# Kernel tuning notes

Hardware: AMD Instinct MI355X
Metric: run time of the kernel (lower is better)

Reference implementation:

```python
import jax, jax.numpy as jnp
import numpy as np
from jax import lax

T = 100
TAU = 2.0
ALPHA = 2.0  # ATan surrogate default
EPS = 1e-5

@jax.custom_vjp
def atan_spike(x):
    return (x >= 0.0).astype(x.dtype)

def _atan_fwd(x):
    return atan_spike(x), x

def _atan_bwd(x, g):
    return (g * (ALPHA / 2.0) / (1.0 + (jnp.pi / 2.0 * ALPHA * x) ** 2),)

atan_spike.defvjp(_atan_fwd, _atan_bwd)

def lif(x_seq):
    # spikingjelly LIFNode: decay_input=True, v_threshold=1, hard reset to 0
    def step(v, x):
        v = v + (x - v) / TAU
        s = atan_spike(v - 1.0)
        return v * (1.0 - s), s
    return lax.scan(step, jnp.zeros_like(x_seq[0]), x_seq)[1]

def conv3x3(x, w):
    return lax.conv_general_dilated(x, w, (1, 1), 'SAME',
                                    dimension_numbers=('NCHW', 'OIHW', 'NCHW'))

def bn(x, g, b, m, v):
    inv = g / jnp.sqrt(v + EPS)
    return x * inv[:, None, None] + (b - m * inv)[:, None, None]

def maxpool2(x):
    return lax.reduce_window(x, -jnp.inf, lax.max, (1, 1, 2, 2), (1, 1, 2, 2), 'VALID')

def setup_inputs() -> dict:
    key = jax.random.key(0)
    ks = jax.random.split(key, 10)
    B, C = 16, 64
    x = jax.random.uniform(ks[0], (B, 1, 28, 28), dtype=jnp.float32)
    W1 = jax.random.normal(ks[1], (C, 1, 3, 3), dtype=jnp.float32) * np.sqrt(2.0 / 9)
    W2 = jax.random.normal(ks[2], (C, C, 3, 3), dtype=jnp.float32) * np.sqrt(2.0 / (9 * C))
    Wfc1 = jax.random.normal(ks[3], (C * 16, C * 49), dtype=jnp.float32) * np.sqrt(2.0 / (C * 49))
    Wfc2 = jax.random.normal(ks[4], (10, C * 16), dtype=jnp.float32) * np.sqrt(2.0 / (C * 16))
    g1 = jnp.ones((C,), jnp.float32); b1 = jnp.zeros((C,), jnp.float32)
    m1 = jax.random.normal(ks[5], (C,), jnp.float32) * 0.1
    v1 = jax.random.uniform(ks[6], (C,), jnp.float32, 0.5, 1.5)
    g2 = jnp.ones((C,), jnp.float32); b2 = jnp.zeros((C,), jnp.float32)
    m2 = jax.random.normal(ks[7], (C,), jnp.float32) * 0.1
    v2 = jax.random.uniform(ks[8], (C,), jnp.float32, 0.5, 1.5)
    return {'x': x, 'W1': W1, 'g1': g1, 'b1': b1, 'm1': m1, 'v1': v1,
            'W2': W2, 'g2': g2, 'b2': b2, 'm2': m2, 'v2': v2,
            'Wfc1': Wfc1, 'Wfc2': Wfc2}

def reference(x, W1, g1, b1, m1, v1, W2, g2, b2, m2, v2, Wfc1, Wfc2):
    B = x.shape[0]
    C = W1.shape[0]
    # conv1+BN1: input identical at every timestep, compute once and broadcast
    h1 = bn(conv3x3(x, W1), g1, b1, m1, v1)                 # [B,C,28,28]
    x_seq = jnp.broadcast_to(h1, (T,) + h1.shape)           # [T,B,C,28,28]
    s1 = lif(x_seq)                                         # [T,B,C,28,28]
    p1 = maxpool2(s1.reshape(T * B, C, 28, 28))             # [T*B,C,14,14]
    h2 = bn(conv3x3(p1, W2), g2, b2, m2, v2).reshape(T, B, C, 14, 14)
    s2 = lif(h2)                                            # [T,B,C,14,14]
    p2 = maxpool2(s2.reshape(T * B, C, 14, 14)).reshape(T, B, C * 49)
    s3 = lif(jnp.einsum('tbi,oi->tbo', p2, Wfc1))           # [T,B,C*16]
    s4 = lif(jnp.einsum('tbi,oi->tbo', s3, Wfc2))           # [T,B,10]
    return s4.mean(axis=0)                                  # [B,10]
```

## Files before the change

### kernel.cpp

```cpp
#include <hip/hip_runtime.h>
#include <hip/hip_bf16.h>

typedef unsigned int uint;
typedef _Float16 f16;
typedef _Float16 f16x8 __attribute__((ext_vector_type(8)));
typedef float f32x4 __attribute__((ext_vector_type(4)));

#define T_STEPS 100

#define OFF_H1    (size_t)0
#define OFF_WHI   (size_t)0
#define OFF_WLO   (size_t)73728
#define OFF_P1    (size_t)3211264
#define OFF_H2    (size_t)29425664
#define OFF_H3    (size_t)29425664
#define OFF_S3    (size_t)35979264
#define OFF_H4    (size_t)37617664
#define OFF_WF1L  (size_t)37681664
#define OFF_P2    (size_t)109707264
#define OFF_WF1H  (size_t)114724864

__device__ __forceinline__ int lif_step_i(float& v, float x) {
  v = __fadd_rn(v, __fmul_rn(__fsub_rn(x, v), 0.5f));
  if (v >= 1.0f) { v = 0.0f; return 1; }
  return 0;
}

__global__ __launch_bounds__(256) void k_prep_w2(const float* __restrict__ w2,
                                                 f16* __restrict__ whi, f16* __restrict__ wlo) {
  int i = blockIdx.x * 256 + threadIdx.x;
  int j = i & 7, l = (i >> 3) & 63, cb = (i >> 9) & 3, kb = i >> 11;
  int k = kb * 32 + (l >> 4) * 8 + j;
  int co = cb * 16 + (l & 15);
  int ci = k & 63, tap = k >> 6;
  int dy = tap / 3, dx = tap - 3 * dy;
  float w = w2[((co * 64 + ci) * 3 + dy) * 3 + dx];
  float hif = (fabsf(w) < 6.104e-5f) ? 0.0f : (float)(f16)w;
  whi[i] = (f16)hif;
  wlo[i] = (f16)((w - hif) * 4096.0f);
}

__global__ __launch_bounds__(256) void k_prep_wfc1(const float* __restrict__ wfc1,
                                                   f16* __restrict__ whi, f16* __restrict__ wlo) {
  int i = blockIdx.x * 256 + threadIdx.x;
  int j = i & 7, lane = (i >> 3) & 63;
  int rest = i >> 9;
  int oblk = rest & 63, kbG = rest >> 6;
  int o = oblk * 16 + (lane & 15);
  int k = kbG * 32 + (lane >> 4) * 8 + j;
  float w = wfc1[(size_t)o * 3136 + k];
  float hif = (fabsf(w) < 6.104e-5f) ? 0.0f : (float)(f16)w;
  whi[i] = (f16)hif;
  wlo[i] = (f16)((w - hif) * 4096.0f);
}

__global__ __launch_bounds__(256) void k_zero_h3(float4* __restrict__ p) {
  p[blockIdx.x * 256 + threadIdx.x] = make_float4(0.f, 0.f, 0.f, 0.f);
}

__global__ __launch_bounds__(256) void k_conv1(const float* __restrict__ x, const float* __restrict__ w1,
                                               const float* __restrict__ g1, const float* __restrict__ b1,
                                               const float* __restrict__ m1, const float* __restrict__ v1,
                                               float* __restrict__ h1) {
  int i = blockIdx.x * 256 + threadIdx.x;
  int pos = i % 784;
  int bc  = i / 784;
  int c = bc & 63, b = bc >> 6;
  int y = pos / 28, xx = pos % 28;
  float a = 0.f;
#pragma unroll
  for (int dy = 0; dy < 3; ++dy) {
    int iy = y + dy - 1;
#pragma unroll
    for (int dx = 0; dx < 3; ++dx) {
      int ix = xx + dx - 1;
      if (iy >= 0 && iy < 28 && ix >= 0 && ix < 28)
        a = fmaf(w1[c * 9 + dy * 3 + dx], x[b * 784 + iy * 28 + ix], a);
    }
  }
  float inv  = g1[c] / sqrtf(v1[c] + 1e-5f);
  float bias = __fsub_rn(b1[c], __fmul_rn(m1[c], inv));
  h1[i] = __fadd_rn(__fmul_rn(a, inv), bias);
}

__global__ __launch_bounds__(256) void k_lif1pool(const float* __restrict__ h1,
                                                  unsigned char* __restrict__ p1) {
  int t = blockIdx.x * 256 + threadIdx.x;
  int ci = t & 63, xx = (t >> 6) & 15, y = (t >> 10) & 15, b = t >> 14;
  int pix = y * 16 + xx;
  size_t outbase = (size_t)b * 16384 + pix * 64 + ci;
  const size_t tstride = (size_t)16 * 16384;
  if (y == 0 || y == 15 || xx == 0 || xx == 15) {
    for (int tt = 0; tt < T_STEPS; ++tt) p1[outbase + (size_t)tt * tstride] = 0;
    return;
  }
  int py = y - 1, px = xx - 1;
  const float* hp = h1 + ((size_t)(b * 64 + ci) * 28 + 2 * py) * 28 + 2 * px;
  float h00 = hp[0], h01 = hp[1], h10 = hp[28], h11 = hp[29];
  float v00 = 0.f, v01 = 0.f, v10 = 0.f, v11 = 0.f;
  for (int tt = 0; tt < T_STEPS; ++tt) {
    int s = 0;
    s |= lif_step_i(v00, h00);
    s |= lif_step_i(v01, h01);
    s |= lif_step_i(v10, h10);
    s |= lif_step_i(v11, h11);
    p1[outbase + (size_t)tt * tstride] = (unsigned char)s;
  }
}

__global__ __launch_bounds__(256, 2) void k_conv2(const unsigned char* __restrict__ p1,
                                                  const f16* __restrict__ whi, const f16* __restrict__ wlo,
                                                  const float* __restrict__ g2, const float* __restrict__ b2,
                                                  const float* __restrict__ m2, const float* __restrict__ v2,
                                                  float* __restrict__ h2) {
  __shared__ unsigned char smem[33024];
  const int tid = threadIdx.x;
  const int tb = blockIdx.x;
  const unsigned char* img = p1 + (size_t)tb * 16384;
#pragma unroll
  for (int it = 0; it < 4; ++it) {
    int s = it * 256 + tid;
    uint4 d = *(const uint4*)(img + (size_t)s * 16);
    int pix = s >> 2, c4 = s & 3;
    uint dw[4] = {d.x, d.y, d.z, d.w};
    f16x8 va, vb;
#pragma unroll
    for (int e = 0; e < 8; ++e) {
      va[e] = (f16)(float)((dw[e >> 2] >> ((e & 3) * 8)) & 255u);
      vb[e] = (f16)(float)((dw[2 + (e >> 2)] >> ((e & 3) * 8)) & 255u);
    }
    int rowbase = pix * 128;
    int sw = (pix & 7) << 4;
    *(f16x8*)(smem + rowbase + ((c4 * 32) ^ sw)) = va;
    *(f16x8*)(smem + rowbase + ((c4 * 32 + 16) ^ sw)) = vb;
  }
  if (tid < 16) *(uint4*)(smem + 32768 + tid * 16) = make_uint4(0u, 0u, 0u, 0u);
  __syncthreads();

  const int lane = tid & 63;
  const int wave = tid >> 6;
  const int ox = lane & 15;
  const int g = lane >> 4;
  const int cohalf = wave & 1;
  const int pb0 = (wave >> 1) * 7;

  f32x4 aH0[7], aL0[7], aH1[7], aL1[7];
#pragma unroll
  for (int q = 0; q < 7; ++q) {
    aH0[q] = (f32x4){0.f, 0.f, 0.f, 0.f};
    aL0[q] = (f32x4){0.f, 0.f, 0.f, 0.f};
    aH1[q] = (f32x4){0.f, 0.f, 0.f, 0.f};
    aL1[q] = (f32x4){0.f, 0.f, 0.f, 0.f};
  }

#pragma unroll 2
  for (int kb = 0; kb < 18; ++kb) {
    const int tap = kb >> 1;
    const int dy = tap / 3, dx = tap - 3 * dy;
    const int cilo2 = (kb & 1) * 64;
    size_t abase = ((size_t)(kb * 4 + cohalf * 2) * 64 + lane) * 8;
    f16x8 ah0 = *(const f16x8*)(whi + abase);
    f16x8 al0 = *(const f16x8*)(wlo + abase);
    f16x8 ah1 = *(const f16x8*)(whi + abase + 512);
    f16x8 al1 = *(const f16x8*)(wlo + abase + 512);
#pragma unroll
    for (int q = 0; q < 7; ++q) {
      int pix = (pb0 + q + dy) * 16 + ox + dx;
      int boff = pix * 128 + ((cilo2 + g * 16) ^ ((pix & 7) << 4));
      f16x8 bf = *(const f16x8*)(smem + boff);
      aH0[q] = __builtin_amdgcn_mfma_f32_16x16x32_f16(ah0, bf, aH0[q], 0, 0, 0);
      aL0[q] = __builtin_amdgcn_mfma_f32_16x16x32_f16(al0, bf, aL0[q], 0, 0, 0);
      aH1[q] = __builtin_amdgcn_mfma_f32_16x16x32_f16(ah1, bf, aH1[q], 0, 0, 0);
      aL1[q] = __builtin_amdgcn_mfma_f32_16x16x32_f16(al1, bf, aL1[q], 0, 0, 0);
    }
  }

  float binv[2][4], bofs[2][4];
#pragma unroll
  for (int cb = 0; cb < 2; ++cb)
#pragma unroll
    for (int r = 0; r < 4; ++r) {
      int co = (cohalf * 2 + cb) * 16 + g * 4 + r;
      float iv = g2[co] / sqrtf(v2[co] + 1e-5f);
      binv[cb][r] = iv;
      bofs[cb][r] = __fsub_rn(b2[co], __fmul_rn(m2[co], iv));
    }

  if (ox < 14) {
#pragma unroll
    for (int q = 0; q < 7; ++q) {
      int oy = pb0 + q;
#pragma unroll
      for (int r = 0; r < 4; ++r) {
        int co0 = cohalf * 32 + g * 4 + r;
        float s0 = __fadd_rn(aH0[q][r], __fmul_rn(aL0[q][r], 1.0f / 4096.0f));
        h2[((size_t)tb * 64 + co0) * 196 + oy * 14 + ox] =
            __fadd_rn(__fmul_rn(s0, binv[0][r]), bofs[0][r]);
        int co1 = co0 + 16;
        float s1 = __fadd_rn(aH1[q][r], __fmul_rn(aL1[q][r], 1.0f / 4096.0f));
        h2[((size_t)tb * 64 + co1) * 196 + oy * 14 + ox] =
            __fadd_rn(__fmul_rn(s1, binv[1][r]), bofs[1][r]);
      }
    }
  }
}

__global__ __launch_bounds__(256) void k_lif2pool(const float* __restrict__ h2,
                                                  unsigned char* __restrict__ p2) {
  int t = blockIdx.x * 256 + threadIdx.x;
  int px = t % 7;
  int r1 = t / 7;
  int py = r1 % 7;
  int r2 = r1 / 7;
  int c = r2 & 63, b = r2 >> 6;
  const float* base = h2 + ((size_t)b * 64 + c) * 196 + (2 * py) * 14 + 2 * px;
  const size_t tstride = (size_t)16 * 64 * 196;
  unsigned char* op = p2 + (size_t)b * 3136 + c * 49 + py * 7 + px;
  const size_t otstride = (size_t)16 * 3136;
  float v00 = 0.f, v01 = 0.f, v10 = 0.f, v11 = 0.f;
#pragma unroll 4
  for (int tt = 0; tt < T_STEPS; ++tt) {
    const float* hp = base + (size_t)tt * tstride;
    float2 r0 = *(const float2*)(hp);
    float2 r1v = *(const float2*)(hp + 14);
    int s = 0;
    s |= lif_step_i(v00, r0.x);
    s |= lif_step_i(v01, r0.y);
    s |= lif_step_i(v10, r1v.x);
    s |= lif_step_i(v11, r1v.y);
    op[(size_t)tt * otstride] = (unsigned char)s;
  }
}

__global__ __launch_bounds__(256, 2) void k_fc1(const unsigned char* __restrict__ p2,
                                                const f16* __restrict__ whi, const f16* __restrict__ wlo,
                                                float* __restrict__ h3) {
  __shared__ unsigned char bsm[2][128 * 80];
  const int tid = threadIdx.x;
  const int lane = tid & 63;
  const int wave = tid >> 6;
  const int tb0 = blockIdx.x * 128;
  const int oblk = blockIdx.y * 4 + wave;
  const int z = blockIdx.z;
  const int tbl = tid >> 1, kslot = tid & 1;
  const int stb = tb0 + tbl;
  const unsigned char* sp = p2 + (size_t)stb * 3136 + z * 1568 + kslot * 16;
  const bool sok = (stb < 1600);

  f32x4 accH[8], accL[8];
#pragma unroll
  for (int n = 0; n < 8; ++n) {
    accH[n] = (f32x4){0.f, 0.f, 0.f, 0.f};
    accL[n] = (f32x4){0.f, 0.f, 0.f, 0.f};
  }

  const int kbG0 = z * 49;
  size_t afrag = ((size_t)(kbG0 * 64 + oblk) * 64 + lane) * 8;
  const size_t astep = (size_t)64 * 64 * 8;
  f16x8 ahC = *(const f16x8*)(whi + afrag);
  f16x8 alC = *(const f16x8*)(wlo + afrag);

  for (int kb = 0; kb < 49; ++kb) {
    uint4 d = make_uint4(0u, 0u, 0u, 0u);
    if (sok) d = *(const uint4*)(sp + kb * 32);
    f16x8 ahN, alN;
    if (kb < 48) {
      ahN = *(const f16x8*)(whi + afrag + (kb + 1) * astep);
      alN = *(const f16x8*)(wlo + afrag + (kb + 1) * astep);
    }
    uint dw[4] = {d.x, d.y, d.z, d.w};
    f16x8 va, vb;
#pragma unroll
    for (int e = 0; e < 8; ++e) {
      va[e] = (f16)(float)((dw[e >> 2] >> ((e & 3) * 8)) & 255u);
      vb[e] = (f16)(float)((dw[2 + (e >> 2)] >> ((e & 3) * 8)) & 255u);
    }
    unsigned char* row = &bsm[kb & 1][tbl * 80];
    *(f16x8*)(row + kslot * 32) = va;
    *(f16x8*)(row + kslot * 32 + 16) = vb;
    __syncthreads();
    const unsigned char* buf = &bsm[kb & 1][0];
#pragma unroll
    for (int n = 0; n < 8; ++n) {
      f16x8 bf = *(const f16x8*)(buf + (n * 16 + (lane & 15)) * 80 + (lane >> 4) * 16);
      accH[n] = __builtin_amdgcn_mfma_f32_16x16x32_f16(ahC, bf, accH[n], 0, 0, 0);
      accL[n] = __builtin_amdgcn_mfma_f32_16x16x32_f16(alC, bf, accL[n], 0, 0, 0);
    }
    ahC = ahN; alC = alN;
  }

  const int o = blockIdx.y * 64 + wave * 16 + (lane >> 4) * 4;
#pragma unroll
  for (int n = 0; n < 8; ++n) {
    int tb = tb0 + n * 16 + (lane & 15);
    if (tb < 1600) {
      float* hp = h3 + (size_t)tb * 1024 + o;
#pragma unroll
      for (int r = 0; r < 4; ++r) {
        float s = __fadd_rn(accH[n][r], __fmul_rn(accL[n][r], 1.0f / 4096.0f));
        atomicAdd(hp + r, s);
      }
    }
  }
}

__global__ __launch_bounds__(256) void k_lif3(const float* __restrict__ h3,
                                              unsigned char* __restrict__ s3) {
  int t = blockIdx.x * 256 + threadIdx.x;
  int o = t & 1023, b = t >> 10;
  size_t base = (size_t)b * 1024 + o;
  float v = 0.f;
#pragma unroll 5
  for (int tt = 0; tt < T_STEPS; ++tt) {
    float xv = h3[base + (size_t)tt * 16384];
    s3[base + (size_t)tt * 16384] = (unsigned char)lif_step_i(v, xv);
  }
}

__global__ __launch_bounds__(64) void k_fc2(const unsigned char* __restrict__ s3,
                                            const float* __restrict__ wfc2,
                                            float* __restrict__ h4) {
  int tb = blockIdx.x;
  int l = threadIdx.x;
  const unsigned char* srow = s3 + (size_t)tb * 1024;
  float p[10];
#pragma unroll
  for (int o = 0; o < 10; ++o) p[o] = 0.f;
  for (int j = 0; j < 16; ++j) {
    int k = l + j * 64;
    float s = (float)srow[k];
#pragma unroll
    for (int o = 0; o < 10; ++o)
      p[o] = fmaf(s, wfc2[o * 1024 + k], p[o]);
  }
#pragma unroll
  for (int o = 0; o < 10; ++o) {
    float v = p[o];
    for (int off = 32; off > 0; off >>= 1) v += __shfl_down(v, off, 64);
    if (l == 0) h4[(size_t)tb * 10 + o] = v;
  }
}

__global__ __launch_bounds__(256) void k_lif4mean(const float* __restrict__ h4,
                                                  float* __restrict__ out) {
  int t = threadIdx.x;
  if (t >= 160) return;
  int o = t % 10, b = t / 10;
  float v = 0.f;
  int cnt = 0;
#pragma unroll 10
  for (int tt = 0; tt < T_STEPS; ++tt) {
    float xv = h4[(size_t)tt * 160 + b * 10 + o];
    cnt += lif_step_i(v, xv);
  }
  out[b * 10 + o] = (float)cnt / 100.0f;
}

extern "C" void kernel_launch(void* const* d_in, const int* in_sizes, int n_in,
                              void* d_out, int out_size, void* d_ws, size_t ws_size,
                              hipStream_t stream) {
  const float* x    = (const float*)d_in[0];
  const float* W1   = (const float*)d_in[1];
  const float* g1   = (const float*)d_in[2];
  const float* b1   = (const float*)d_in[3];
  const float* m1   = (const float*)d_in[4];
  const float* v1   = (const float*)d_in[5];
  const float* W2   = (const float*)d_in[6];
  const float* g2   = (const float*)d_in[7];
  const float* b2   = (const float*)d_in[8];
  const float* m2   = (const float*)d_in[9];
  const float* v2   = (const float*)d_in[10];
  const float* Wfc1 = (const float*)d_in[11];
  const float* Wfc2 = (const float*)d_in[12];
  float* out = (float*)d_out;
  char* ws = (char*)d_ws;

  float*         h1   = (float*)(ws + OFF_H1);
  f16*           whi  = (f16*)(ws + OFF_WHI);
  f16*           wlo  = (f16*)(ws + OFF_WLO);
  unsigned char* p1   = (unsigned char*)(ws + OFF_P1);
  float*         h2   = (float*)(ws + OFF_H2);
  unsigned char* p2   = (unsigned char*)(ws + OFF_P2);
  float*         h3   = (float*)(ws + OFF_H3);
  unsigned char* s3   = (unsigned char*)(ws + OFF_S3);
  float*         h4   = (float*)(ws + OFF_H4);
  f16*           wf1h = (f16*)(ws + OFF_WF1H);
  f16*           wf1l = (f16*)(ws + OFF_WF1L);

  k_conv1<<<3136, 256, 0, stream>>>(x, W1, g1, b1, m1, v1, h1);
  k_lif1pool<<<1024, 256, 0, stream>>>(h1, p1);
  k_prep_w2<<<144, 256, 0, stream>>>(W2, whi, wlo);
  k_conv2<<<1600, 256, 0, stream>>>(p1, whi, wlo, g2, b2, m2, v2, h2);
  k_lif2pool<<<196, 256, 0, stream>>>(h2, p2);
  k_prep_wfc1<<<12544, 256, 0, stream>>>(Wfc1, wf1h, wf1l);
  k_zero_h3<<<1600, 256, 0, stream>>>((float4*)h3);
  dim3 gfc1(13, 16, 2);
  k_fc1<<<gfc1, 256, 0, stream>>>(p2, wf1h, wf1l, h3);
  k_lif3<<<64, 256, 0, stream>>>(h3, s3);
  k_fc2<<<1600, 64, 0, stream>>>(s3, Wfc2, h4);
  k_lif4mean<<<1, 256, 0, stream>>>(h4, out);
}
```

Baseline: 278.6 us.

## Store pooled spikes as f16, prefetch fc1 activations, remap fc1 grid

The layer-2 LIF/pool kernel now writes spikes directly as f16, so fc1 no longer unpacks bytes to half before staging them in LDS. fc1 now software-prefetches the next k-block's activations into registers, runs on a flattened 1D grid whose blocks are grouped so neighbouring blocks share output/k slices, and raises its occupancy hint to 3 blocks per CU. The spike buffer doubles in size, so workspace offsets are moved. The lif3 unroll factor is also increased.

```diff
diff --git a/kernel.cpp b/kernel.cpp
--- a/kernel.cpp
+++ b/kernel.cpp
@@ -17,8 +17,8 @@
 #define OFF_S3    (size_t)35979264
 #define OFF_H4    (size_t)37617664
 #define OFF_WF1L  (size_t)37681664
-#define OFF_P2    (size_t)109707264
-#define OFF_WF1H  (size_t)114724864
+#define OFF_WF1H  (size_t)44104192
+#define OFF_P2H   (size_t)109707264
 
 __device__ __forceinline__ int lif_step_i(float& v, float x) {
   v = __fadd_rn(v, __fmul_rn(__fsub_rn(x, v), 0.5f));
@@ -206,7 +206,7 @@
 }
 
 __global__ __launch_bounds__(256) void k_lif2pool(const float* __restrict__ h2,
-                                                  unsigned char* __restrict__ p2) {
+                                                  f16* __restrict__ p2h) {
   int t = blockIdx.x * 256 + threadIdx.x;
   int px = t % 7;
   int r1 = t / 7;
@@ -215,7 +215,7 @@
   int c = r2 & 63, b = r2 >> 6;
   const float* base = h2 + ((size_t)b * 64 + c) * 196 + (2 * py) * 14 + 2 * px;
   const size_t tstride = (size_t)16 * 64 * 196;
-  unsigned char* op = p2 + (size_t)b * 3136 + c * 49 + py * 7 + px;
+  f16* op = p2h + (size_t)b * 3136 + c * 49 + py * 7 + px;
   const size_t otstride = (size_t)16 * 3136;
   float v00 = 0.f, v01 = 0.f, v10 = 0.f, v11 = 0.f;
 #pragma unroll 4
@@ -228,24 +228,28 @@
     s |= lif_step_i(v01, r0.y);
     s |= lif_step_i(v10, r1v.x);
     s |= lif_step_i(v11, r1v.y);
-    op[(size_t)tt * otstride] = (unsigned char)s;
-  }
-}
-
-__global__ __launch_bounds__(256, 2) void k_fc1(const unsigned char* __restrict__ p2,
+    op[(size_t)tt * otstride] = (f16)s;
+  }
+}
+
+__global__ __launch_bounds__(256, 3) void k_fc1(const f16* __restrict__ p2h,
                                                 const f16* __restrict__ whi, const f16* __restrict__ wlo,
                                                 float* __restrict__ h3) {
   __shared__ unsigned char bsm[2][128 * 80];
   const int tid = threadIdx.x;
   const int lane = tid & 63;
   const int wave = tid >> 6;
-  const int tb0 = blockIdx.x * 128;
-  const int oblk = blockIdx.y * 4 + wave;
-  const int z = blockIdx.z;
-  const int tbl = tid >> 1, kslot = tid & 1;
+  int bid = blockIdx.x;
+  int k8 = bid & 7, j = bid >> 3;
+  int sh = j / 13, xb = j - sh * 13;
+  int s = k8 + 8 * sh;
+  int yb = s >> 1, z = s & 1;
+  const int tb0 = xb * 128;
+  const int oblk = yb * 4 + wave;
+  const int tbl = tid >> 1, half = tid & 1;
   const int stb = tb0 + tbl;
-  const unsigned char* sp = p2 + (size_t)stb * 3136 + z * 1568 + kslot * 16;
   const bool sok = (stb < 1600);
+  const uint4* spq = (const uint4*)(p2h + (size_t)stb * 3136 + z * 1568 + half * 16);
 
   f32x4 accH[8], accL[8];
 #pragma unroll
@@ -259,25 +263,21 @@
   const size_t astep = (size_t)64 * 64 * 8;
   f16x8 ahC = *(const f16x8*)(whi + afrag);
   f16x8 alC = *(const f16x8*)(wlo + afrag);
+  const uint4 z4 = make_uint4(0u, 0u, 0u, 0u);
+  uint4 dA = sok ? spq[0] : z4;
+  uint4 dB = sok ? spq[1] : z4;
 
   for (int kb = 0; kb < 49; ++kb) {
-    uint4 d = make_uint4(0u, 0u, 0u, 0u);
-    if (sok) d = *(const uint4*)(sp + kb * 32);
-    f16x8 ahN, alN;
+    uint4 nA = z4, nB = z4;
+    f16x8 ahN = ahC, alN = alC;
     if (kb < 48) {
-      ahN = *(const f16x8*)(whi + afrag + (kb + 1) * astep);
-      alN = *(const f16x8*)(wlo + afrag + (kb + 1) * astep);
-    }
-    uint dw[4] = {d.x, d.y, d.z, d.w};
-    f16x8 va, vb;
-#pragma unroll
-    for (int e = 0; e < 8; ++e) {
-      va[e] = (f16)(float)((dw[e >> 2] >> ((e & 3) * 8)) & 255u);
-      vb[e] = (f16)(float)((dw[2 + (e >> 2)] >> ((e & 3) * 8)) & 255u);
-    }
-    unsigned char* row = &bsm[kb & 1][tbl * 80];
-    *(f16x8*)(row + kslot * 32) = va;
-    *(f16x8*)(row + kslot * 32 + 16) = vb;
+      if (sok) { nA = spq[kb * 4 + 4]; nB = spq[kb * 4 + 5]; }
+      ahN = *(const f16x8*)(whi + afrag + (size_t)(kb + 1) * astep);
+      alN = *(const f16x8*)(wlo + afrag + (size_t)(kb + 1) * astep);
+    }
+    unsigned char* row = &bsm[kb & 1][tbl * 80 + half * 32];
+    *(uint4*)(row) = dA;
+    *(uint4*)(row + 16) = dB;
     __syncthreads();
     const unsigned char* buf = &bsm[kb & 1][0];
 #pragma unroll
@@ -286,10 +286,10 @@
       accH[n] = __builtin_amdgcn_mfma_f32_16x16x32_f16(ahC, bf, accH[n], 0, 0, 0);
       accL[n] = __builtin_amdgcn_mfma_f32_16x16x32_f16(alC, bf, accL[n], 0, 0, 0);
     }
-    ahC = ahN; alC = alN;
-  }
-
-  const int o = blockIdx.y * 64 + wave * 16 + (lane >> 4) * 4;
+    dA = nA; dB = nB; ahC = ahN; alC = alN;
+  }
+
+  const int o = yb * 64 + wave * 16 + (lane >> 4) * 4;
 #pragma unroll
   for (int n = 0; n < 8; ++n) {
     int tb = tb0 + n * 16 + (lane & 15);
@@ -297,8 +297,8 @@
       float* hp = h3 + (size_t)tb * 1024 + o;
 #pragma unroll
       for (int r = 0; r < 4; ++r) {
-        float s = __fadd_rn(accH[n][r], __fmul_rn(accL[n][r], 1.0f / 4096.0f));
-        atomicAdd(hp + r, s);
+        float sv = __fadd_rn(accH[n][r], __fmul_rn(accL[n][r], 1.0f / 4096.0f));
+        atomicAdd(hp + r, sv);
       }
     }
   }
@@ -310,7 +310,7 @@
   int o = t & 1023, b = t >> 10;
   size_t base = (size_t)b * 1024 + o;
   float v = 0.f;
-#pragma unroll 5
+#pragma unroll 10
   for (int tt = 0; tt < T_STEPS; ++tt) {
     float xv = h3[base + (size_t)tt * 16384];
     s3[base + (size_t)tt * 16384] = (unsigned char)lif_step_i(v, xv);
@@ -380,7 +380,7 @@
   f16*           wlo  = (f16*)(ws + OFF_WLO);
   unsigned char* p1   = (unsigned char*)(ws + OFF_P1);
   float*         h2   = (float*)(ws + OFF_H2);
-  unsigned char* p2   = (unsigned char*)(ws + OFF_P2);
+  f16*           p2h  = (f16*)(ws + OFF_P2H);
   float*         h3   = (float*)(ws + OFF_H3);
   unsigned char* s3   = (unsigned char*)(ws + OFF_S3);
   float*         h4   = (float*)(ws + OFF_H4);
@@ -391,11 +391,10 @@
   k_lif1pool<<<1024, 256, 0, stream>>>(h1, p1);
   k_prep_w2<<<144, 256, 0, stream>>>(W2, whi, wlo);
   k_conv2<<<1600, 256, 0, stream>>>(p1, whi, wlo, g2, b2, m2, v2, h2);
-  k_lif2pool<<<196, 256, 0, stream>>>(h2, p2);
+  k_lif2pool<<<196, 256, 0, stream>>>(h2, p2h);
   k_prep_wfc1<<<12544, 256, 0, stream>>>(Wfc1, wf1h, wf1l);
   k_zero_h3<<<1600, 256, 0, stream>>>((float4*)h3);
-  dim3 gfc1(13, 16, 2);
-  k_fc1<<<gfc1, 256, 0, stream>>>(p2, wf1h, wf1l, h3);
+  k_fc1<<<416, 256, 0, stream>>>(p2h, wf1h, wf1l, h3);
   k_lif3<<<64, 256, 0, stream>>>(h3, s3);
   k_fc2<<<1600, 64, 0, stream>>>(s3, Wfc2, h4);
   k_lif4mean<<<1, 256, 0, stream>>>(h4, out);
```

Measured after the change: 280.3 us. About the same (+0.6%).
